# Performance work log

Hardware: AMD Instinct MI355X
Metric: run time of the kernel (lower is better)

## Reference

```python
import jax, jax.numpy as jnp
import numpy as np
import math

B, T, D = 4, 4096, 256


def setup_inputs() -> dict:
    key = jax.random.key(0)
    ks = jax.random.split(key, 12)
    stdv = 1.0 / math.sqrt(D)
    u = lambda k, shape, s: jax.random.uniform(k, shape, jnp.float32, -s, s)
    return {
        "query": jax.random.normal(ks[0], (B, T, D), jnp.float32),
        "value": jax.random.normal(ks[1], (B, T, D), jnp.float32),
        # gate vectors, init uniform(-1/sqrt(D), 1/sqrt(D)) per reset_parameters
        "q_vec": u(ks[2], (D,), stdv),
        "k_vec": u(ks[3], (D,), stdv),
        "v_vec": u(ks[4], (D,), stdv),
        # nn.Linear params (torch default init: uniform(-1/sqrt(fan_in), ...))
        "Wq": u(ks[5], (D, D), stdv), "bq": u(ks[6], (D,), stdv),
        "Ws": u(ks[7], (D, D), stdv), "bs": u(ks[8], (D,), stdv),
        "Wt": u(ks[9], (D, D), stdv), "bt": u(ks[10], (D,), stdv),
    }


def reference(query, value, q_vec, k_vec, v_vec, Wq, bq, Ws, bs, Wt, bt):
    d = query.shape[-1]
    # q = Linear(query) * sigmoid(query_vector)
    q = (jnp.einsum('btd,ed->bte', query, Wq) + bq) * jax.nn.sigmoid(q_vec)
    # k = value * sigmoid(key_vector)
    k = value * jax.nn.sigmoid(k_vec)
    # v gate: infer=False branch -> GLU-style gate of sigmoid(value_vector)
    vv = jax.nn.sigmoid(v_vec)
    v_gate = jax.nn.sigmoid(Ws @ vv + bs) * jnp.tanh(Wt @ vv + bt)
    v = value * v_gate
    # scores [B, T, T]
    w = jnp.einsum('bqd,bkd->bqk', q, k) / jnp.sqrt(jnp.float32(d))
    # causal: multiply by tril mask then replace exact zeros with -inf
    # (faithful to the original's weight[weight==0]=-inf quirk)
    Tn = w.shape[-1]
    tril = jnp.tril(jnp.ones((Tn, Tn), w.dtype))
    w = w * tril
    w = jnp.where(w == 0.0, -jnp.inf, w)
    attn = jax.nn.softmax(w, axis=-1)
    return jnp.einsum('bqk,bkd->bqd', attn, v)
```

## Files before the change

### kernel.cpp

```cpp
#include <hip/hip_runtime.h>
#include <math.h>

#define D 256
#define T 4096
#define KT (17408/2)
#define VT (20480/2)
#define PSTR ((size_t)4*T*D)

typedef __attribute__((ext_vector_type(8))) short bf16x8;
typedef __attribute__((ext_vector_type(4))) float f32x4;
typedef __attribute__((ext_vector_type(4))) unsigned short u16x4;

__device__ __forceinline__ unsigned short f2bf(float x){
  unsigned int u = __float_as_uint(x);
  unsigned int r = (u + 0x7FFFu + ((u >> 16) & 1u)) >> 16;
  return (unsigned short)r;
}
__device__ __forceinline__ float bf2f(unsigned short h){
  return __uint_as_float(((unsigned int)h) << 16);
}

__device__ __forceinline__ void gl_lds16(const void* g, void* l){
  __builtin_amdgcn_global_load_lds((const __attribute__((address_space(1))) unsigned int*)g,
                                   (__attribute__((address_space(3))) unsigned int*)l, 16, 0, 0);
}

__global__ __launch_bounds__(256) void prep_kernel(
    const float* __restrict__ q_vec, const float* __restrict__ k_vec,
    const float* __restrict__ v_vec, const float* __restrict__ Ws,
    const float* __restrict__ bs, const float* __restrict__ Wt,
    const float* __restrict__ bt, const float* __restrict__ Wq,
    float* __restrict__ gates, unsigned short* __restrict__ wq_g){
  int t = threadIdx.x;
  if(blockIdx.x == 0){
    __shared__ float vv[D];
    vv[t]         = 1.f/(1.f + __expf(-v_vec[t]));
    gates[t]      = 1.f/(1.f + __expf(-q_vec[t]));
    gates[D + t]  = 1.f/(1.f + __expf(-k_vec[t]));
    __syncthreads();
    const f32x4* wsr = (const f32x4*)(Ws + (size_t)t*D);
    const f32x4* wtr = (const f32x4*)(Wt + (size_t)t*D);
    const f32x4* vvv = (const f32x4*)vv;
    f32x4 a0 = {0,0,0,0}, a1 = {0,0,0,0}, c0 = {0,0,0,0}, c1 = {0,0,0,0};
    for(int i=0;i<64;i+=2){
      f32x4 v0 = vvv[i], v1 = vvv[i+1];
      a0 += wsr[i]*v0; a1 += wsr[i+1]*v1;
      c0 += wtr[i]*v0; c1 += wtr[i+1]*v1;
    }
    f32x4 as = a0 + a1, cs = c0 + c1;
    float s1 = bs[t] + as[0]+as[1]+as[2]+as[3];
    float s2 = bt[t] + cs[0]+cs[1]+cs[2]+cs[3];
    gates[2*D + t] = (1.f/(1.f + __expf(-s1))) * tanhf(s2);
  } else {
    int kc = blockIdx.x - 1;
    const float* src = Wq + (size_t)t*D + kc*32;
    unsigned short* dst = wq_g + (size_t)kc*10240 + t*40;
    #pragma unroll
    for(int u=0;u<4;u++){
      bf16x8 pk;
      #pragma unroll
      for(int x=0;x<8;x++) pk[x] = (short)f2bf(src[u*8+x]);
      *(bf16x8*)&dst[u*8] = pk;
    }
  }
}

__global__ __launch_bounds__(256) void mid_kernel(
    const float* __restrict__ query, const unsigned short* __restrict__ wq_g,
    const float* __restrict__ bq, const float* __restrict__ gates,
    unsigned short* __restrict__ q_g,
    const float* __restrict__ value,
    unsigned short* __restrict__ k_g, unsigned short* __restrict__ vt_g){
  __shared__ __align__(16) unsigned short smem[2][10240];
  int tid = threadIdx.x;
  if(blockIdx.x < 256){
    int w = tid >> 6; int l = tid & 63;
    int lr = l & 15, lc = l >> 4;
    int r0 = blockIdx.x * 64;
    f32x4 acc[16];
    #pragma unroll
    for(int n=0;n<16;n++) acc[n] = (f32x4){0.f,0.f,0.f,0.f};
    const float* qrow = query + (size_t)(r0 + w*16 + lr)*D;
    #pragma unroll
    for(int i=0;i<5;i++){ int c = i*256 + tid; gl_lds16(wq_g + c*8, (char*)smem[0] + c*16); }
    __syncthreads();
    int cur = 0;
    for(int kc=0; kc<8; kc++){
      if(kc < 7){
        #pragma unroll
        for(int i=0;i<5;i++){ int c = i*256 + tid;
          gl_lds16(wq_g + (size_t)(kc+1)*10240 + c*8, (char*)smem[cur^1] + c*16); }
      }
      bf16x8 af;
      {
        const float* s = qrow + kc*32 + lc*8;
        #pragma unroll
        for(int x=0;x<8;x++) af[x] = (short)f2bf(s[x]);
      }
      #pragma unroll
      for(int n=0;n<16;n++){
        bf16x8 bfrag = *(const bf16x8*)&smem[cur][(n*16 + lr)*40 + lc*8];
        acc[n] = __builtin_amdgcn_mfma_f32_16x16x32_bf16(af, bfrag, acc[n], 0, 0, 0);
      }
      __syncthreads();
      cur ^= 1;
    }
    #pragma unroll
    for(int n=0;n<16;n++){
      int col = n*16 + lr;
      float bb = bq[col], gg = gates[col];
      #pragma unroll
      for(int r=0;r<4;r++){
        int row = r0 + w*16 + lc*4 + r;
        q_g[(size_t)row*D + col] = f2bf((acc[n][r] + bb) * gg);
      }
    }
  } else {
    int bid2 = blockIdx.x - 256;
    int b = bid2 >> 7, jt = bid2 & 127;
    const float* vbase = value + ((size_t)b*T + jt*32)*D;
    const float* gk = gates + D;
    const float* vg = gates + 2*D;
    unsigned short* kt = k_g  + (size_t)bid2 * KT;
    unsigned short* vt = vt_g + (size_t)bid2 * VT;
    #pragma unroll
    for(int i=0;i<4;i++){
      int g = i*256 + tid; int j = g >> 5, c = g & 31;
      const float* src = vbase + j*D + c*8;
      bf16x8 pk;
      #pragma unroll
      for(int x=0;x<8;x++) pk[x] = (short)f2bf(src[x] * gk[c*8+x]);
      *(bf16x8*)&kt[j*264 + c*8] = pk;
    }
    float* lds = (float*)smem;
    for(int c=0;c<4;c++){
      __syncthreads();
      {
        int row = tid >> 3, cg = tid & 7;
        const float* src = vbase + (size_t)row*D + c*64 + cg*8;
        f32x4 v0 = *(const f32x4*)src;
        f32x4 v1 = *(const f32x4*)(src + 4);
        *(f32x4*)&lds[row*68 + cg*8]     = v0;
        *(f32x4*)&lds[row*68 + cg*8 + 4] = v1;
      }
      __syncthreads();
      {
        int d0l = tid >> 2, u = tid & 3;
        int d0 = c*64 + d0l;
        float gd = vg[d0];
        bf16x8 pk;
        #pragma unroll
        for(int x=0;x<8;x++){
          int p = u*8 + x;
          int ksrc = ((p>>3)<<2) + (p&3) + (((p>>2)&1)<<4);
          pk[x] = (short)f2bf(lds[ksrc*68 + d0l] * gd);
        }
        *(bf16x8*)&vt[d0*40 + u*8] = pk;
      }
    }
  }
}

__global__ __launch_bounds__(512, 4) void flash_kernel(
    const unsigned short* __restrict__ q_g,
    const unsigned short* __restrict__ k_g,
    const unsigned short* __restrict__ vt_g,
    unsigned short* __restrict__ parts,
    float* __restrict__ ml, int logS){
  __shared__ __align__(16) unsigned short kbuf[2][KT];
  __shared__ __align__(16) unsigned short vbuf[2][VT];
  int tid = threadIdx.x; int w = tid >> 6, l = tid & 63;
  int lr = l & 15, lc = l >> 4;
  int S = 1 << logS;
  int bid = blockIdx.x;
  int x = bid & 7; int b = x >> 1; int p = x & 1;
  int item = (bid >> 3)*2 + p;
  int rblk = 31 - (item >> logS);
  int s = item & (S - 1);
  int r0 = rblk * 128;
  int wrow0 = r0 + w*16;
  int nt = 4*rblk + 4;
  int jt0 = (s*nt) >> logS, jt1 = ((s+1)*nt) >> logS;
  int gr = wrow0 + lr;

  bf16x8 qf[8];
  {
    const unsigned short* qbase = q_g + ((size_t)b*T + wrow0 + lr)*D + lc*8;
    #pragma unroll
    for(int kc=0;kc<8;kc++) qf[kc] = *(const bf16x8*)(qbase + kc*32);
  }
  f32x4 o[16];
  #pragma unroll
  for(int n=0;n<16;n++) o[n] = (f32x4){0.f,0.f,0.f,0.f};
  float m = -INFINITY, lsum = 0.f;

  const unsigned short* ktb = k_g  + (size_t)b*128*KT;
  const unsigned short* vtb = vt_g + (size_t)b*128*VT;

  if(jt1 > jt0){
    const unsigned short* ks = ktb + (size_t)jt0*KT;
    const unsigned short* vs = vtb + (size_t)jt0*VT;
    for(int c=w; c<37; c+=8){
      if(c < 17) gl_lds16(ks + c*512 + l*8, (char*)kbuf[jt0&1] + c*1024);
      else       gl_lds16(vs + (c-17)*512 + l*8, (char*)vbuf[jt0&1] + (c-17)*1024);
    }
  }

  for(int jt=jt0; jt<jt1; jt++){
    int cur = jt & 1;
    asm volatile("s_waitcnt vmcnt(0)" ::: "memory");
    __builtin_amdgcn_s_barrier();
    __builtin_amdgcn_sched_barrier(0);
    if(jt+1 < jt1){
      const unsigned short* ks = ktb + (size_t)(jt+1)*KT;
      const unsigned short* vs = vtb + (size_t)(jt+1)*VT;
      for(int c=w; c<37; c+=8){
        if(c < 17) gl_lds16(ks + c*512 + l*8, (char*)kbuf[cur^1] + c*1024);
        else       gl_lds16(vs + (c-17)*512 + l*8, (char*)vbuf[cur^1] + (c-17)*1024);
      }
    }
    int j0 = jt*32;
    bool active = (j0 <= wrow0 + 15);
    if(active){
      f32x4 s0 = {0,0,0,0}, s1 = {0,0,0,0};
      __builtin_amdgcn_s_setprio(1);
      #pragma unroll
      for(int kc=0;kc<8;kc++){
        bf16x8 k0 = *(const bf16x8*)&kbuf[cur][lr*264        + (kc*4 + lc)*8];
        bf16x8 k1 = *(const bf16x8*)&kbuf[cur][(16 + lr)*264 + (kc*4 + lc)*8];
        s0 = __builtin_amdgcn_mfma_f32_16x16x32_bf16(k0, qf[kc], s0, 0,0,0);
        s1 = __builtin_amdgcn_mfma_f32_16x16x32_bf16(k1, qf[kc], s1, 0,0,0);
      }
      __builtin_amdgcn_s_setprio(0);
      float sv0[4], sv1[4];
      #pragma unroll
      for(int r=0;r<4;r++){
        float x0 = s0[r]*0.0625f; int gj0 = j0 + lc*4 + r;
        float x1 = s1[r]*0.0625f; int gj1 = gj0 + 16;
        if(gj0 > gr || x0 == 0.0f) x0 = -INFINITY;
        if(gj1 > gr || x1 == 0.0f) x1 = -INFINITY;
        sv0[r]=x0; sv1[r]=x1;
      }
      float pmax = fmaxf(fmaxf(fmaxf(sv0[0],sv0[1]),fmaxf(sv0[2],sv0[3])),
                         fmaxf(fmaxf(sv1[0],sv1[1]),fmaxf(sv1[2],sv1[3])));
      pmax = fmaxf(pmax, __shfl_xor(pmax, 16));
      pmax = fmaxf(pmax, __shfl_xor(pmax, 32));
      bool mv = (pmax > m + 8.0f);
      float mn = mv ? pmax : m;
      float alpha = mv ? __expf(m - mn) : 1.0f;
      float p0[4], p1[4];
      #pragma unroll
      for(int r=0;r<4;r++){
        p0[r] = (sv0[r] == -INFINITY) ? 0.f : __expf(sv0[r] - mn);
        p1[r] = (sv1[r] == -INFINITY) ? 0.f : __expf(sv1[r] - mn);
      }
      unsigned long long anymv = __builtin_amdgcn_ballot_w64(mv);
      if(anymv){
        float a0 = __shfl(alpha, lc*4 + 0);
        float a1 = __shfl(alpha, lc*4 + 1);
        float a2 = __shfl(alpha, lc*4 + 2);
        float a3 = __shfl(alpha, lc*4 + 3);
        #pragma unroll
        for(int n=0;n<16;n++){
          o[n][0] *= a0; o[n][1] *= a1; o[n][2] *= a2; o[n][3] *= a3;
        }
      }
      float ps = ((p0[0]+p0[1])+(p0[2]+p0[3])) + ((p1[0]+p1[1])+(p1[2]+p1[3]));
      lsum = lsum*alpha + ps;
      m = mn;
      bf16x8 pa;
      #pragma unroll
      for(int r=0;r<4;r++){ pa[r] = (short)f2bf(p0[r]); pa[4+r] = (short)f2bf(p1[r]); }
      __builtin_amdgcn_s_setprio(1);
      #pragma unroll
      for(int n=0;n<16;n++){
        bf16x8 vf = *(const bf16x8*)&vbuf[cur][(n*16 + lr)*40 + lc*8];
        o[n] = __builtin_amdgcn_mfma_f32_16x16x32_bf16(pa, vf, o[n], 0,0,0);
      }
      __builtin_amdgcn_s_setprio(0);
    }
  }

  unsigned short* obase = parts + (size_t)s*PSTR + ((size_t)b*T + wrow0)*D;
  #pragma unroll
  for(int r=0;r<4;r++){
    #pragma unroll
    for(int n=0;n<16;n++){
      obase[(size_t)(lc*4 + r)*D + n*16 + lr] = f2bf(o[n][r]);
    }
  }
  lsum += __shfl_xor(lsum, 16);
  lsum += __shfl_xor(lsum, 32);
  if(l < 16){
    float* mlb = ml + ((size_t)s*4*T + (size_t)b*T + wrow0 + lr)*2;
    mlb[0] = m; mlb[1] = lsum;
  }
}

__global__ __launch_bounds__(256) void combine_kernel(
    const unsigned short* __restrict__ parts, const float* __restrict__ ml,
    float* __restrict__ out, int S){
  size_t idx = (size_t)blockIdx.x*256 + threadIdx.x;
  size_t e = idx*4;
  size_t row = e >> 8;
  float mm = -INFINITY;
  for(int s=0;s<S;s++) mm = fmaxf(mm, ml[((size_t)s*4*T + row)*2]);
  float denom = 0.f;
  f32x4 acc = {0.f,0.f,0.f,0.f};
  for(int s=0;s<S;s++){
    float ms = ml[((size_t)s*4*T + row)*2];
    float ls = ml[((size_t)s*4*T + row)*2 + 1];
    float as = __expf(ms - mm);
    denom += as*ls;
    u16x4 v = *(const u16x4*)&parts[(size_t)s*PSTR + e];
    #pragma unroll
    for(int xx=0;xx<4;xx++) acc[xx] += as*bf2f(v[xx]);
  }
  float inv = 1.0f/denom;
  f32x4 r;
  #pragma unroll
  for(int xx=0;xx<4;xx++) r[xx] = acc[xx]*inv;
  *(f32x4*)&out[e] = r;
}

extern "C" void kernel_launch(void* const* d_in, const int* in_sizes, int n_in,
                              void* d_out, int out_size, void* d_ws, size_t ws_size,
                              hipStream_t stream){
  (void)in_sizes; (void)n_in; (void)out_size;
  const float* query = (const float*)d_in[0];
  const float* value = (const float*)d_in[1];
  const float* q_vec = (const float*)d_in[2];
  const float* k_vec = (const float*)d_in[3];
  const float* v_vec = (const float*)d_in[4];
  const float* Wq    = (const float*)d_in[5];
  const float* bq    = (const float*)d_in[6];
  const float* Ws    = (const float*)d_in[7];
  const float* bs    = (const float*)d_in[8];
  const float* Wt    = (const float*)d_in[9];
  const float* bt    = (const float*)d_in[10];
  char* ws = (char*)d_ws;
  unsigned short* q_g  = (unsigned short*)(ws);
  unsigned short* k_g  = (unsigned short*)(ws + 8388608);
  unsigned short* vt_g = (unsigned short*)(ws + 17301504);
  unsigned short* wq_g = (unsigned short*)(ws + 27787264);
  float* gates         = (float*)(ws + 27951104);
  unsigned short* parts= (unsigned short*)(ws + 27955200);
  float* out = (float*)d_out;

  size_t base = 27955200;
  size_t mlsz = (size_t)8*4*T*2*4;
  int logS;
  if(ws_size >= base + 8*PSTR*2 + mlsz)      logS = 3;
  else if(ws_size >= base + 4*PSTR*2 + mlsz) logS = 2;
  else                                       logS = 1;
  int S = 1 << logS;
  float* ml = (float*)(ws + base + (size_t)S*PSTR*2);

  hipLaunchKernelGGL(prep_kernel, dim3(9),   dim3(256), 0, stream,
                     q_vec, k_vec, v_vec, Ws, bs, Wt, bt, Wq, gates, wq_g);
  hipLaunchKernelGGL(mid_kernel,  dim3(768), dim3(256), 0, stream,
                     query, wq_g, bq, gates, q_g, value, k_g, vt_g);
  hipLaunchKernelGGL(flash_kernel, dim3(128*S), dim3(512), 0, stream,
                     q_g, k_g, vt_g, parts, ml, logS);
  hipLaunchKernelGGL(combine_kernel, dim3((4*T*D/4)/256), dim3(256), 0, stream,
                     parts, ml, out, S);
}
```

Before: 130.0 us.

## Remap split work items, split QK accumulators, drop setprio, skip empty partials

Changes how block IDs map to (row-block, split) pairs so that the two parity blocks take different halves of the split range. Splits the QK^T MFMA chain into two independent accumulator pairs to shorten the dependency chain. Removes s_setprio around both MFMA loops. In the combine kernel, caches the m/l values in registers and skips loading partials whose scale underflows to zero, which saves bandwidth but adds a branch and a fixed-size array limited to S<=8.

Measured after the change: 134.3 us. 1.03x slower.

```diff
diff --git a/kernel.cpp b/kernel.cpp
--- a/kernel.cpp
+++ b/kernel.cpp
@@ -174,9 +174,10 @@
   int S = 1 << logS;
   int bid = blockIdx.x;
   int x = bid & 7; int b = x >> 1; int p = x & 1;
-  int item = (bid >> 3)*2 + p;
-  int rblk = 31 - (item >> logS);
-  int s = item & (S - 1);
+  int item = bid >> 3;
+  int half = S >> 1;
+  int rblk = 31 - (item / half);
+  int s = p*half + (item & (half - 1));
   int r0 = rblk * 128;
   int wrow0 = r0 + w*16;
   int nt = 4*rblk + 4;
@@ -222,16 +223,19 @@
     int j0 = jt*32;
     bool active = (j0 <= wrow0 + 15);
     if(active){
-      f32x4 s0 = {0,0,0,0}, s1 = {0,0,0,0};
-      __builtin_amdgcn_s_setprio(1);
-      #pragma unroll
-      for(int kc=0;kc<8;kc++){
+      f32x4 s0a = {0,0,0,0}, s0b = {0,0,0,0}, s1a = {0,0,0,0}, s1b = {0,0,0,0};
+      #pragma unroll
+      for(int kc=0;kc<4;kc++){
         bf16x8 k0 = *(const bf16x8*)&kbuf[cur][lr*264        + (kc*4 + lc)*8];
         bf16x8 k1 = *(const bf16x8*)&kbuf[cur][(16 + lr)*264 + (kc*4 + lc)*8];
-        s0 = __builtin_amdgcn_mfma_f32_16x16x32_bf16(k0, qf[kc], s0, 0,0,0);
-        s1 = __builtin_amdgcn_mfma_f32_16x16x32_bf16(k1, qf[kc], s1, 0,0,0);
-      }
-      __builtin_amdgcn_s_setprio(0);
+        bf16x8 k0h = *(const bf16x8*)&kbuf[cur][lr*264        + ((kc+4)*4 + lc)*8];
+        bf16x8 k1h = *(const bf16x8*)&kbuf[cur][(16 + lr)*264 + ((kc+4)*4 + lc)*8];
+        s0a = __builtin_amdgcn_mfma_f32_16x16x32_bf16(k0,  qf[kc],   s0a, 0,0,0);
+        s1a = __builtin_amdgcn_mfma_f32_16x16x32_bf16(k1,  qf[kc],   s1a, 0,0,0);
+        s0b = __builtin_amdgcn_mfma_f32_16x16x32_bf16(k0h, qf[kc+4], s0b, 0,0,0);
+        s1b = __builtin_amdgcn_mfma_f32_16x16x32_bf16(k1h, qf[kc+4], s1b, 0,0,0);
+      }
+      f32x4 s0 = s0a + s0b, s1 = s1a + s1b;
       float sv0[4], sv1[4];
       #pragma unroll
       for(int r=0;r<4;r++){
@@ -271,13 +275,11 @@
       bf16x8 pa;
       #pragma unroll
       for(int r=0;r<4;r++){ pa[r] = (short)f2bf(p0[r]); pa[4+r] = (short)f2bf(p1[r]); }
-      __builtin_amdgcn_s_setprio(1);
       #pragma unroll
       for(int n=0;n<16;n++){
         bf16x8 vf = *(const bf16x8*)&vbuf[cur][(n*16 + lr)*40 + lc*8];
         o[n] = __builtin_amdgcn_mfma_f32_16x16x32_bf16(pa, vf, o[n], 0,0,0);
       }
-      __builtin_amdgcn_s_setprio(0);
     }
   }
 
@@ -303,18 +305,23 @@
   size_t idx = (size_t)blockIdx.x*256 + threadIdx.x;
   size_t e = idx*4;
   size_t row = e >> 8;
+  float msv[8], lsv[8];
   float mm = -INFINITY;
-  for(int s=0;s<S;s++) mm = fmaxf(mm, ml[((size_t)s*4*T + row)*2]);
+  for(int s=0;s<S;s++){
+    msv[s] = ml[((size_t)s*4*T + row)*2];
+    lsv[s] = ml[((size_t)s*4*T + row)*2 + 1];
+    mm = fmaxf(mm, msv[s]);
+  }
   float denom = 0.f;
   f32x4 acc = {0.f,0.f,0.f,0.f};
   for(int s=0;s<S;s++){
-    float ms = ml[((size_t)s*4*T + row)*2];
-    float ls = ml[((size_t)s*4*T + row)*2 + 1];
-    float as = __expf(ms - mm);
-    denom += as*ls;
-    u16x4 v = *(const u16x4*)&parts[(size_t)s*PSTR + e];
-    #pragma unroll
-    for(int xx=0;xx<4;xx++) acc[xx] += as*bf2f(v[xx]);
+    float as = __expf(msv[s] - mm);
+    if(as != 0.0f){
+      denom += as*lsv[s];
+      u16x4 v = *(const u16x4*)&parts[(size_t)s*PSTR + e];
+      #pragma unroll
+      for(int xx=0;xx<4;xx++) acc[xx] += as*bf2f(v[xx]);
+    }
   }
   float inv = 1.0f/denom;
   f32x4 r;
```
